# Kernel tuning notes

Measured on AMD Instinct MI355X. Metric: run time of the kernel, lower is better.

The kernel has to match this reference:

```python
import jax, jax.numpy as jnp
import numpy as np

E, B, DS, DA, H = 8, 16384, 32, 8, 128
SLOPE = 0.01  # torch leaky_relu default


def setup_inputs() -> dict:
    key = jax.random.key(0)
    ks = jax.random.split(key, 6)
    din = DS + DA
    return {
        "states": jax.random.normal(ks[0], (E, B, DS), jnp.float32),
        "actions": jax.random.normal(ks[1], (E, B, DA), jnp.float32),
        "W0": jax.random.normal(ks[2], (E, din, H), jnp.float32) / np.sqrt(din),
        "b0": jnp.zeros((E, H), jnp.float32),
        "W1": jax.random.normal(ks[3], (E, H, H), jnp.float32) / np.sqrt(H),
        "b1": jnp.zeros((E, H), jnp.float32),
        "W2": jax.random.normal(ks[4], (E, H, DS), jnp.float32) / np.sqrt(H),
        "b2": jnp.zeros((E, DS), jnp.float32),
    }


def reference(states, actions, W0, b0, W1, b1, W2, b2):
    # inp: (E_in, B, din); each input slice i is evaluated by every member j
    inp = jnp.concatenate([states, actions], axis=2)
    h = jax.nn.leaky_relu(
        jnp.einsum("ibd,jdh->ijbh", inp, W0) + b0[None, :, None, :], SLOPE
    )
    h = jax.nn.leaky_relu(
        jnp.einsum("ijbh,jhk->ijbk", h, W1) + b1[None, :, None, :], SLOPE
    )
    preds = jnp.einsum("ijbh,jhk->ijbk", h, W2) + b2[None, :, None, :]  # (E,E,B,DS)
    delta_mean = preds.mean(axis=0)           # (E, B, DS)
    var = preds.var(axis=0, ddof=1)           # torch.var default is unbiased
    next_state_mean = delta_mean + states
    return next_state_mean, var
```

## Files before the change

### kernel.cpp

```cpp
#include <hip/hip_runtime.h>
#include <hip/hip_bf16.h>


#define NE 8
#define NB 16384
#define DS 32
#define DA 8
#define HH 128
#define DIN 40
#define BT 64
#define SLOPE 0.01f

using bf16x8 = __attribute__((ext_vector_type(8))) short;
using f32x4  = __attribute__((ext_vector_type(4))) float;

__device__ __forceinline__ unsigned short f2bf(float f) {
    unsigned int u = __float_as_uint(f);
    u += 0x7FFFu + ((u >> 16) & 1u);
    return (unsigned short)(u >> 16);
}

__device__ __forceinline__ float lrelu(float x) { return fmaxf(x, SLOPE * x); }

__device__ __forceinline__ unsigned int pack2bf(float a, float b) {
    union { __hip_bfloat162 h; unsigned int u; } cv;
    cv.h = __float22bfloat162_rn(make_float2(a, b));
    return cv.u;
}

__device__ __forceinline__ int sin_idx(int row, int kb) {
    return row * 64 + ((kb ^ (row & 7)) << 3);
}
__device__ __forceinline__ int sh_idx(int row, int kb) {
    return row * 128 + ((kb ^ (row & 15)) << 3);
}

__global__ __launch_bounds__(256, 3)
void ens_mlp_kernel(const float* __restrict__ states,
                    const float* __restrict__ actions,
                    const float* __restrict__ W0g,
                    const float* __restrict__ b0g,
                    const float* __restrict__ W1g,
                    const float* __restrict__ b1g,
                    const float* __restrict__ W2g,
                    const float* __restrict__ b2g,
                    float* __restrict__ out)
{
    __shared__ __align__(16) unsigned short sIn[BT * 64];
    __shared__ __align__(16) unsigned short sHa[BT * 128];
    __shared__ __align__(16) unsigned short sHb[BT * 128];

    const int j    = blockIdx.x & 7;
    const int bt   = blockIdx.x >> 3;
    const int b0   = bt * BT;
    const int tid  = threadIdx.x;
    const int wave = tid >> 6;
    const int lane = tid & 63;
    const int q    = lane >> 4;
    const int l16  = lane & 15;
    const int fb   = 32 * wave;
    const int l2m  = 32 * (wave >> 1);
    const int l2n  = 16 * (wave & 1);

    {
        uint4 z; z.x = z.y = z.z = z.w = 0u;
        uint4* p = reinterpret_cast<uint4*>(&sIn[tid * 32]);
        p[0] = z; p[1] = z; p[2] = z; p[3] = z;
    }

    const float* W0j = W0g + j * (DIN * HH);
    const float* W1j = W1g + j * (HH * HH);
    const float* W2j = W2g + j * (HH * DS);

    bf16x8 w0f[2][2];
    bf16x8 w1f[4][2];
    bf16x8 w2f[4];
    float b1r[2][4];
    float b2s;

    #pragma unroll
    for (int ks = 0; ks < 2; ++ks)
      #pragma unroll
      for (int mt = 0; mt < 2; ++mt) {
        const int n = fb + mt * 16 + l16;
        #pragma unroll
        for (int t = 0; t < 8; ++t) {
          const int k = ks * 32 + q * 8 + t;
          const float v = (k < DIN) ? W0j[k * HH + n]
                        : (k == DIN ? b0g[j * HH + n] : 0.f);
          w0f[ks][mt][t] = (short)f2bf(v);
        }
      }
    #pragma unroll
    for (int ks = 0; ks < 4; ++ks)
      #pragma unroll
      for (int mt = 0; mt < 2; ++mt) {
        const int n = fb + mt * 16 + l16;
        #pragma unroll
        for (int t = 0; t < 8; ++t) {
          const int k = ks * 32 + q * 8 + t;
          w1f[ks][mt][t] = (short)f2bf(W1j[k * HH + n]);
        }
      }
    #pragma unroll
    for (int ks = 0; ks < 4; ++ks) {
        const int n = l2n + l16;
        #pragma unroll
        for (int t = 0; t < 8; ++t) {
          const int k = ks * 32 + q * 8 + t;
          w2f[ks][t] = (short)f2bf(W2j[k * DS + n]);
        }
    }
    #pragma unroll
    for (int mt = 0; mt < 2; ++mt)
      #pragma unroll
      for (int r = 0; r < 4; ++r)
        b1r[mt][r] = b1g[j * HH + fb + mt * 16 + q * 4 + r];
    b2s = b2g[j * DS + l2n + l16];

    float sa[2][4], sq[2][4];
    #pragma unroll
    for (int mt = 0; mt < 2; ++mt)
      #pragma unroll
      for (int r = 0; r < 4; ++r) { sa[mt][r] = 0.f; sq[mt][r] = 0.f; }

    const f32x4 z4 = {0.f, 0.f, 0.f, 0.f};

    const int srow = tid >> 2;
    const int scb  = tid & 3;
    const int soff = srow * DS + scb * 8;
    unsigned short* const sdst = &sIn[sin_idx(srow, scb)];
    unsigned short* const adst = &sIn[sin_idx(lane, 4)];

    __syncthreads();

    if (tid < BT) sIn[sin_idx(tid, 5)] = 0x3F80;

    {
        const float4* sp = reinterpret_cast<const float4*>(states + (size_t)b0 * DS + soff);
        const float4 f0 = sp[0], f1 = sp[1];
        uint4 pk;
        pk.x = pack2bf(f0.x, f0.y); pk.y = pack2bf(f0.z, f0.w);
        pk.z = pack2bf(f1.x, f1.y); pk.w = pack2bf(f1.z, f1.w);
        *reinterpret_cast<uint4*>(sdst) = pk;
        if (tid < BT) {
            const float4* ap = reinterpret_cast<const float4*>(actions + ((size_t)b0 + lane) * DA);
            const float4 a0 = ap[0], a1 = ap[1];
            uint4 apk;
            apk.x = pack2bf(a0.x, a0.y); apk.y = pack2bf(a0.z, a0.w);
            apk.z = pack2bf(a1.x, a1.y); apk.w = pack2bf(a1.z, a1.w);
            *reinterpret_cast<uint4*>(adst) = apk;
        }
    }
    __syncthreads();

    for (int i = 0; i < NE; ++i) {
        #pragma unroll
        for (int nh = 0; nh < 2; ++nh) {
            f32x4 acc[2][2];
            #pragma unroll
            for (int mt = 0; mt < 2; ++mt)
              #pragma unroll
              for (int nt = 0; nt < 2; ++nt) acc[mt][nt] = z4;
            #pragma unroll
            for (int ks = 0; ks < 2; ++ks) {
                bf16x8 bf[2];
                #pragma unroll
                for (int nt = 0; nt < 2; ++nt) {
                    const int row = nh * 32 + nt * 16 + l16;
                    bf[nt] = *(const bf16x8*)(&sIn[sin_idx(row, ks * 4 + q)]);
                }
                #pragma unroll
                for (int mt = 0; mt < 2; ++mt)
                  #pragma unroll
                  for (int nt = 0; nt < 2; ++nt)
                    acc[mt][nt] = __builtin_amdgcn_mfma_f32_16x16x32_bf16(
                        w0f[ks][mt], bf[nt], acc[mt][nt], 0, 0, 0);
            }
            #pragma unroll
            for (int mt = 0; mt < 2; ++mt)
              #pragma unroll
              for (int nt = 0; nt < 2; ++nt) {
                const int row = nh * 32 + nt * 16 + l16;
                const int blk = (fb >> 3) + mt * 2 + (q >> 1);
                const int idx = sh_idx(row, blk) + (q & 1) * 4;
                const float v0 = lrelu(acc[mt][nt][0]);
                const float v1 = lrelu(acc[mt][nt][1]);
                const float v2 = lrelu(acc[mt][nt][2]);
                const float v3 = lrelu(acc[mt][nt][3]);
                uint2 pk; pk.x = pack2bf(v0, v1); pk.y = pack2bf(v2, v3);
                *reinterpret_cast<uint2*>(&sHa[idx]) = pk;
              }
        }
        __syncthreads();

        if (i < NE - 1) {
            const float4* sp = reinterpret_cast<const float4*>(
                states + ((size_t)(i + 1) * NB + b0) * DS + soff);
            const float4 f0 = sp[0], f1 = sp[1];
            uint4 pk;
            pk.x = pack2bf(f0.x, f0.y); pk.y = pack2bf(f0.z, f0.w);
            pk.z = pack2bf(f1.x, f1.y); pk.w = pack2bf(f1.z, f1.w);
            *reinterpret_cast<uint4*>(sdst) = pk;
            if (tid < BT) {
                const float4* ap = reinterpret_cast<const float4*>(
                    actions + ((size_t)(i + 1) * NB + b0 + lane) * DA);
                const float4 a0 = ap[0], a1 = ap[1];
                uint4 apk;
                apk.x = pack2bf(a0.x, a0.y); apk.y = pack2bf(a0.z, a0.w);
                apk.z = pack2bf(a1.x, a1.y); apk.w = pack2bf(a1.z, a1.w);
                *reinterpret_cast<uint4*>(adst) = apk;
            }
        }

        #pragma unroll
        for (int nh = 0; nh < 2; ++nh) {
            f32x4 acc[2][2];
            #pragma unroll
            for (int mt = 0; mt < 2; ++mt)
              #pragma unroll
              for (int nt = 0; nt < 2; ++nt) acc[mt][nt] = z4;
            #pragma unroll
            for (int ks = 0; ks < 4; ++ks) {
                bf16x8 bf[2];
                #pragma unroll
                for (int nt = 0; nt < 2; ++nt) {
                    const int row = nh * 32 + nt * 16 + l16;
                    bf[nt] = *(const bf16x8*)(&sHa[sh_idx(row, ks * 4 + q)]);
                }
                #pragma unroll
                for (int mt = 0; mt < 2; ++mt)
                  #pragma unroll
                  for (int nt = 0; nt < 2; ++nt)
                    acc[mt][nt] = __builtin_amdgcn_mfma_f32_16x16x32_bf16(
                        w1f[ks][mt], bf[nt], acc[mt][nt], 0, 0, 0);
            }
            #pragma unroll
            for (int mt = 0; mt < 2; ++mt)
              #pragma unroll
              for (int nt = 0; nt < 2; ++nt) {
                const int row = nh * 32 + nt * 16 + l16;
                const int blk = (fb >> 3) + mt * 2 + (q >> 1);
                const int idx = sh_idx(row, blk) + (q & 1) * 4;
                const float v0 = lrelu(acc[mt][nt][0] + b1r[mt][0]);
                const float v1 = lrelu(acc[mt][nt][1] + b1r[mt][1]);
                const float v2 = lrelu(acc[mt][nt][2] + b1r[mt][2]);
                const float v3 = lrelu(acc[mt][nt][3] + b1r[mt][3]);
                uint2 pk; pk.x = pack2bf(v0, v1); pk.y = pack2bf(v2, v3);
                *reinterpret_cast<uint2*>(&sHb[idx]) = pk;
              }
        }
        __syncthreads();

        {
            f32x4 acc2[2];
            acc2[0] = z4; acc2[1] = z4;
            #pragma unroll
            for (int ks = 0; ks < 4; ++ks) {
                #pragma unroll
                for (int mt = 0; mt < 2; ++mt) {
                    const int row = l2m + 16 * mt + l16;
                    const bf16x8 a2 = *(const bf16x8*)(&sHb[sh_idx(row, ks * 4 + q)]);
                    acc2[mt] = __builtin_amdgcn_mfma_f32_16x16x32_bf16(
                        a2, w2f[ks], acc2[mt], 0, 0, 0);
                }
            }
            #pragma unroll
            for (int mt = 0; mt < 2; ++mt)
              #pragma unroll
              for (int r = 0; r < 4; ++r) {
                const float a = acc2[mt][r];
                sa[mt][r] += a;
                sq[mt][r] = fmaf(a, a, sq[mt][r]);
              }
        }
    }

    #pragma unroll
    for (int mt = 0; mt < 2; ++mt)
      #pragma unroll
      for (int r = 0; r < 4; ++r) {
        const int row = l2m + 16 * mt + q * 4 + r;
        const int col = l2n + l16;
        const size_t o = ((size_t)j * NB + b0 + row) * DS + col;
        const float b  = b2s;
        const float s  = sa[mt][r] + 8.f * b;
        const float s2 = sq[mt][r] + 2.f * b * sa[mt][r] + 8.f * b * b;
        out[o] = s * 0.125f + states[o];
        out[(size_t)NE * NB * DS + o] = (s2 - s * s * 0.125f) * (1.0f / 7.0f);
      }
}

extern "C" void kernel_launch(void* const* d_in, const int* in_sizes, int n_in,
                              void* d_out, int out_size, void* d_ws, size_t ws_size,
                              hipStream_t stream) {
    (void)in_sizes; (void)n_in; (void)d_ws; (void)ws_size; (void)out_size;
    const float* states  = (const float*)d_in[0];
    const float* actions = (const float*)d_in[1];
    const float* W0 = (const float*)d_in[2];
    const float* b0 = (const float*)d_in[3];
    const float* W1 = (const float*)d_in[4];
    const float* b1 = (const float*)d_in[5];
    const float* W2 = (const float*)d_in[6];
    const float* b2 = (const float*)d_in[7];
    float* out = (float*)d_out;
    dim3 grid(NE * (NB / BT));
    ens_mlp_kernel<<<grid, dim3(256), 0, stream>>>(states, actions, W0, b0, W1, b1, W2, b2, out);
}
```

Before: 161.7 us.

## Make blocks persistent over batch tiles and fold biases into accumulator init

The grid shrinks to 96 slots per ensemble member, and each block loops over several 64-row batch tiles. Per-member weights are converted to bf16 register fragments once per block and reused across tiles, which amortises the strided global weight loads and conversions that every block previously paid. The b0 and b1 biases now initialise the MFMA accumulators, replacing the ones-column trick for b0 and the per-element add for b1. In exchange, fewer blocks are in flight, and the tile count may not divide evenly across slots, which can leave a load-imbalance tail. The zero-initialisation of the input tile now has no barrier before other threads write into it, so correctness depends on the shared-memory layout.

Measured after the change: 153.9 us. 1.05x faster.

```diff
diff --git a/kernel.cpp b/kernel.cpp
--- a/kernel.cpp
+++ b/kernel.cpp
@@ -9,6 +9,7 @@
 #define HH 128
 #define DIN 40
 #define BT 64
+#define NSLOT 96
 #define SLOPE 0.01f
 
 using bf16x8 = __attribute__((ext_vector_type(8))) short;
@@ -51,8 +52,7 @@
     __shared__ __align__(16) unsigned short sHb[BT * 128];
 
     const int j    = blockIdx.x & 7;
-    const int bt   = blockIdx.x >> 3;
-    const int b0   = bt * BT;
+    const int slot = blockIdx.x >> 3;
     const int tid  = threadIdx.x;
     const int wave = tid >> 6;
     const int lane = tid & 63;
@@ -75,7 +75,7 @@
     bf16x8 w0f[2][2];
     bf16x8 w1f[4][2];
     bf16x8 w2f[4];
-    float b1r[2][4];
+    f32x4 b0v[2], b1v[2];
     float b2s;
 
     #pragma unroll
@@ -86,9 +86,7 @@
         #pragma unroll
         for (int t = 0; t < 8; ++t) {
           const int k = ks * 32 + q * 8 + t;
-          const float v = (k < DIN) ? W0j[k * HH + n]
-                        : (k == DIN ? b0g[j * HH + n] : 0.f);
-          w0f[ks][mt][t] = (short)f2bf(v);
+          w0f[ks][mt][t] = (short)((k < DIN) ? f2bf(W0j[k * HH + n]) : 0);
         }
       }
     #pragma unroll
@@ -114,15 +112,11 @@
     #pragma unroll
     for (int mt = 0; mt < 2; ++mt)
       #pragma unroll
-      for (int r = 0; r < 4; ++r)
-        b1r[mt][r] = b1g[j * HH + fb + mt * 16 + q * 4 + r];
+      for (int r = 0; r < 4; ++r) {
+        b0v[mt][r] = b0g[j * HH + fb + mt * 16 + q * 4 + r];
+        b1v[mt][r] = b1g[j * HH + fb + mt * 16 + q * 4 + r];
+      }
     b2s = b2g[j * DS + l2n + l16];
-
-    float sa[2][4], sq[2][4];
-    #pragma unroll
-    for (int mt = 0; mt < 2; ++mt)
-      #pragma unroll
-      for (int r = 0; r < 4; ++r) { sa[mt][r] = 0.f; sq[mt][r] = 0.f; }
 
     const f32x4 z4 = {0.f, 0.f, 0.f, 0.f};
 
@@ -132,71 +126,12 @@
     unsigned short* const sdst = &sIn[sin_idx(srow, scb)];
     unsigned short* const adst = &sIn[sin_idx(lane, 4)];
 
-    __syncthreads();
-
-    if (tid < BT) sIn[sin_idx(tid, 5)] = 0x3F80;
-
-    {
-        const float4* sp = reinterpret_cast<const float4*>(states + (size_t)b0 * DS + soff);
-        const float4 f0 = sp[0], f1 = sp[1];
-        uint4 pk;
-        pk.x = pack2bf(f0.x, f0.y); pk.y = pack2bf(f0.z, f0.w);
-        pk.z = pack2bf(f1.x, f1.y); pk.w = pack2bf(f1.z, f1.w);
-        *reinterpret_cast<uint4*>(sdst) = pk;
-        if (tid < BT) {
-            const float4* ap = reinterpret_cast<const float4*>(actions + ((size_t)b0 + lane) * DA);
-            const float4 a0 = ap[0], a1 = ap[1];
-            uint4 apk;
-            apk.x = pack2bf(a0.x, a0.y); apk.y = pack2bf(a0.z, a0.w);
-            apk.z = pack2bf(a1.x, a1.y); apk.w = pack2bf(a1.z, a1.w);
-            *reinterpret_cast<uint4*>(adst) = apk;
-        }
-    }
-    __syncthreads();
-
-    for (int i = 0; i < NE; ++i) {
-        #pragma unroll
-        for (int nh = 0; nh < 2; ++nh) {
-            f32x4 acc[2][2];
-            #pragma unroll
-            for (int mt = 0; mt < 2; ++mt)
-              #pragma unroll
-              for (int nt = 0; nt < 2; ++nt) acc[mt][nt] = z4;
-            #pragma unroll
-            for (int ks = 0; ks < 2; ++ks) {
-                bf16x8 bf[2];
-                #pragma unroll
-                for (int nt = 0; nt < 2; ++nt) {
-                    const int row = nh * 32 + nt * 16 + l16;
-                    bf[nt] = *(const bf16x8*)(&sIn[sin_idx(row, ks * 4 + q)]);
-                }
-                #pragma unroll
-                for (int mt = 0; mt < 2; ++mt)
-                  #pragma unroll
-                  for (int nt = 0; nt < 2; ++nt)
-                    acc[mt][nt] = __builtin_amdgcn_mfma_f32_16x16x32_bf16(
-                        w0f[ks][mt], bf[nt], acc[mt][nt], 0, 0, 0);
-            }
-            #pragma unroll
-            for (int mt = 0; mt < 2; ++mt)
-              #pragma unroll
-              for (int nt = 0; nt < 2; ++nt) {
-                const int row = nh * 32 + nt * 16 + l16;
-                const int blk = (fb >> 3) + mt * 2 + (q >> 1);
-                const int idx = sh_idx(row, blk) + (q & 1) * 4;
-                const float v0 = lrelu(acc[mt][nt][0]);
-                const float v1 = lrelu(acc[mt][nt][1]);
-                const float v2 = lrelu(acc[mt][nt][2]);
-                const float v3 = lrelu(acc[mt][nt][3]);
-                uint2 pk; pk.x = pack2bf(v0, v1); pk.y = pack2bf(v2, v3);
-                *reinterpret_cast<uint2*>(&sHa[idx]) = pk;
-              }
-        }
-        __syncthreads();
-
-        if (i < NE - 1) {
+    for (int bt = slot; bt < NB / BT; bt += NSLOT) {
+        const int b0 = bt * BT;
+
+        {
             const float4* sp = reinterpret_cast<const float4*>(
-                states + ((size_t)(i + 1) * NB + b0) * DS + soff);
+                states + (size_t)b0 * DS + soff);
             const float4 f0 = sp[0], f1 = sp[1];
             uint4 pk;
             pk.x = pack2bf(f0.x, f0.y); pk.y = pack2bf(f0.z, f0.w);
@@ -204,7 +139,7 @@
             *reinterpret_cast<uint4*>(sdst) = pk;
             if (tid < BT) {
                 const float4* ap = reinterpret_cast<const float4*>(
-                    actions + ((size_t)(i + 1) * NB + b0 + lane) * DA);
+                    actions + ((size_t)b0 + lane) * DA);
                 const float4 a0 = ap[0], a1 = ap[1];
                 uint4 apk;
                 apk.x = pack2bf(a0.x, a0.y); apk.y = pack2bf(a0.z, a0.w);
@@ -212,83 +147,150 @@
                 *reinterpret_cast<uint4*>(adst) = apk;
             }
         }
-
-        #pragma unroll
-        for (int nh = 0; nh < 2; ++nh) {
-            f32x4 acc[2][2];
+        __syncthreads();
+
+        float sa[2][4], sq[2][4];
+        #pragma unroll
+        for (int mt = 0; mt < 2; ++mt)
+          #pragma unroll
+          for (int r = 0; r < 4; ++r) { sa[mt][r] = 0.f; sq[mt][r] = 0.f; }
+
+        for (int i = 0; i < NE; ++i) {
             #pragma unroll
-            for (int mt = 0; mt < 2; ++mt)
-              #pragma unroll
-              for (int nt = 0; nt < 2; ++nt) acc[mt][nt] = z4;
+            for (int nh = 0; nh < 2; ++nh) {
+                f32x4 acc[2][2];
+                #pragma unroll
+                for (int mt = 0; mt < 2; ++mt)
+                  #pragma unroll
+                  for (int nt = 0; nt < 2; ++nt) acc[mt][nt] = b0v[mt];
+                #pragma unroll
+                for (int ks = 0; ks < 2; ++ks) {
+                    bf16x8 bf[2];
+                    #pragma unroll
+                    for (int nt = 0; nt < 2; ++nt) {
+                        const int row = nh * 32 + nt * 16 + l16;
+                        bf[nt] = *(const bf16x8*)(&sIn[sin_idx(row, ks * 4 + q)]);
+                    }
+                    #pragma unroll
+                    for (int mt = 0; mt < 2; ++mt)
+                      #pragma unroll
+                      for (int nt = 0; nt < 2; ++nt)
+                        acc[mt][nt] = __builtin_amdgcn_mfma_f32_16x16x32_bf16(
+                            w0f[ks][mt], bf[nt], acc[mt][nt], 0, 0, 0);
+                }
+                #pragma unroll
+                for (int mt = 0; mt < 2; ++mt)
+                  #pragma unroll
+                  for (int nt = 0; nt < 2; ++nt) {
+                    const int row = nh * 32 + nt * 16 + l16;
+                    const int blk = (fb >> 3) + mt * 2 + (q >> 1);
+                    const int idx = sh_idx(row, blk) + (q & 1) * 4;
+                    const float v0 = lrelu(acc[mt][nt][0]);
+                    const float v1 = lrelu(acc[mt][nt][1]);
+                    const float v2 = lrelu(acc[mt][nt][2]);
+                    const float v3 = lrelu(acc[mt][nt][3]);
+                    uint2 pk; pk.x = pack2bf(v0, v1); pk.y = pack2bf(v2, v3);
+                    *reinterpret_cast<uint2*>(&sHa[idx]) = pk;
+                  }
+            }
+            __syncthreads();
+
+            if (i < NE - 1) {
+                const float4* sp = reinterpret_cast<const float4*>(
+                    states + ((size_t)(i + 1) * NB + b0) * DS + soff);
+                const float4 f0 = sp[0], f1 = sp[1];
+                uint4 pk;
+                pk.x = pack2bf(f0.x, f0.y); pk.y = pack2bf(f0.z, f0.w);
+                pk.z = pack2bf(f1.x, f1.y); pk.w = pack2bf(f1.z, f1.w);
+                *reinterpret_cast<uint4*>(sdst) = pk;
+                if (tid < BT) {
+                    const float4* ap = reinterpret_cast<const float4*>(
+                        actions + ((size_t)(i + 1) * NB + b0 + lane) * DA);
+                    const float4 a0 = ap[0], a1 = ap[1];
+                    uint4 apk;
+                    apk.x = pack2bf(a0.x, a0.y); apk.y = pack2bf(a0.z, a0.w);
+                    apk.z = pack2bf(a1.x, a1.y); apk.w = pack2bf(a1.z, a1.w);
+                    *reinterpret_cast<uint4*>(adst) = apk;
+                }
+            }
+
             #pragma unroll
-            for (int ks = 0; ks < 4; ++ks) {
-                bf16x8 bf[2];
-                #pragma unroll
-                for (int nt = 0; nt < 2; ++nt) {
+            for (int nh = 0; nh < 2; ++nh) {
+                f32x4 acc[2][2];
+                #pragma unroll
+                for (int mt = 0; mt < 2; ++mt)
+                  #pragma unroll
+                  for (int nt = 0; nt < 2; ++nt) acc[mt][nt] = b1v[mt];
+                #pragma unroll
+                for (int ks = 0; ks < 4; ++ks) {
+                    bf16x8 bf[2];
+                    #pragma unroll
+                    for (int nt = 0; nt < 2; ++nt) {
+                        const int row = nh * 32 + nt * 16 + l16;
+                        bf[nt] = *(const bf16x8*)(&sHa[sh_idx(row, ks * 4 + q)]);
+                    }
+                    #pragma unroll
+                    for (int mt = 0; mt < 2; ++mt)
+                      #pragma unroll
+                      for (int nt = 0; nt < 2; ++nt)
+                        acc[mt][nt] = __builtin_amdgcn_mfma_f32_16x16x32_bf16(
+                            w1f[ks][mt], bf[nt], acc[mt][nt], 0, 0, 0);
+                }
+                #pragma unroll
+                for (int mt = 0; mt < 2; ++mt)
+                  #pragma unroll
+                  for (int nt = 0; nt < 2; ++nt) {
                     const int row = nh * 32 + nt * 16 + l16;
-                    bf[nt] = *(const bf16x8*)(&sHa[sh_idx(row, ks * 4 + q)]);
+                    const int blk = (fb >> 3) + mt * 2 + (q >> 1);
+                    const int idx = sh_idx(row, blk) + (q & 1) * 4;
+                    const float v0 = lrelu(acc[mt][nt][0]);
+                    const float v1 = lrelu(acc[mt][nt][1]);
+                    const float v2 = lrelu(acc[mt][nt][2]);
+                    const float v3 = lrelu(acc[mt][nt][3]);
+                    uint2 pk; pk.x = pack2bf(v0, v1); pk.y = pack2bf(v2, v3);
+                    *reinterpret_cast<uint2*>(&sHb[idx]) = pk;
+                  }
+            }
+            __syncthreads();
+
+            {
+                f32x4 acc2[2];
+                acc2[0] = z4; acc2[1] = z4;
+                #pragma unroll
+                for (int ks = 0; ks < 4; ++ks) {
+                    #pragma unroll
+                    for (int mt = 0; mt < 2; ++mt) {
+                        const int row = l2m + 16 * mt + l16;
+                        const bf16x8 a2 = *(const bf16x8*)(&sHb[sh_idx(row, ks * 4 + q)]);
+                        acc2[mt] = __builtin_amdgcn_mfma_f32_16x16x32_bf16(
+                            a2, w2f[ks], acc2[mt], 0, 0, 0);
+                    }
                 }
                 #pragma unroll
                 for (int mt = 0; mt < 2; ++mt)
                   #pragma unroll
-                  for (int nt = 0; nt < 2; ++nt)
-                    acc[mt][nt] = __builtin_amdgcn_mfma_f32_16x16x32_bf16(
-                        w1f[ks][mt], bf[nt], acc[mt][nt], 0, 0, 0);
-            }
-            #pragma unroll
-            for (int mt = 0; mt < 2; ++mt)
-              #pragma unroll
-              for (int nt = 0; nt < 2; ++nt) {
-                const int row = nh * 32 + nt * 16 + l16;
-                const int blk = (fb >> 3) + mt * 2 + (q >> 1);
-                const int idx = sh_idx(row, blk) + (q & 1) * 4;
-                const float v0 = lrelu(acc[mt][nt][0] + b1r[mt][0]);
-                const float v1 = lrelu(acc[mt][nt][1] + b1r[mt][1]);
-                const float v2 = lrelu(acc[mt][nt][2] + b1r[mt][2]);
-                const float v3 = lrelu(acc[mt][nt][3] + b1r[mt][3]);
-                uint2 pk; pk.x = pack2bf(v0, v1); pk.y = pack2bf(v2, v3);
-                *reinterpret_cast<uint2*>(&sHb[idx]) = pk;
-              }
-        }
-        __syncthreads();
-
-        {
-            f32x4 acc2[2];
-            acc2[0] = z4; acc2[1] = z4;
-            #pragma unroll
-            for (int ks = 0; ks < 4; ++ks) {
-                #pragma unroll
-                for (int mt = 0; mt < 2; ++mt) {
-                    const int row = l2m + 16 * mt + l16;
-                    const bf16x8 a2 = *(const bf16x8*)(&sHb[sh_idx(row, ks * 4 + q)]);
-                    acc2[mt] = __builtin_amdgcn_mfma_f32_16x16x32_bf16(
-                        a2, w2f[ks], acc2[mt], 0, 0, 0);
-                }
-            }
-            #pragma unroll
-            for (int mt = 0; mt < 2; ++mt)
-              #pragma unroll
-              for (int r = 0; r < 4; ++r) {
-                const float a = acc2[mt][r];
-                sa[mt][r] += a;
-                sq[mt][r] = fmaf(a, a, sq[mt][r]);
-              }
-        }
+                  for (int r = 0; r < 4; ++r) {
+                    const float a = acc2[mt][r];
+                    sa[mt][r] += a;
+                    sq[mt][r] = fmaf(a, a, sq[mt][r]);
+                  }
+            }
+        }
+
+        #pragma unroll
+        for (int mt = 0; mt < 2; ++mt)
+          #pragma unroll
+          for (int r = 0; r < 4; ++r) {
+            const int row = l2m + 16 * mt + q * 4 + r;
+            const int col = l2n + l16;
+            const size_t o = ((size_t)j * NB + b0 + row) * DS + col;
+            const float b  = b2s;
+            const float s  = sa[mt][r] + 8.f * b;
+            const float s2 = sq[mt][r] + 2.f * b * sa[mt][r] + 8.f * b * b;
+            out[o] = s * 0.125f + states[o];
+            out[(size_t)NE * NB * DS + o] = (s2 - s * s * 0.125f) * (1.0f / 7.0f);
+          }
     }
-
-    #pragma unroll
-    for (int mt = 0; mt < 2; ++mt)
-      #pragma unroll
-      for (int r = 0; r < 4; ++r) {
-        const int row = l2m + 16 * mt + q * 4 + r;
-        const int col = l2n + l16;
-        const size_t o = ((size_t)j * NB + b0 + row) * DS + col;
-        const float b  = b2s;
-        const float s  = sa[mt][r] + 8.f * b;
-        const float s2 = sq[mt][r] + 2.f * b * sa[mt][r] + 8.f * b * b;
-        out[o] = s * 0.125f + states[o];
-        out[(size_t)NE * NB * DS + o] = (s2 - s * s * 0.125f) * (1.0f / 7.0f);
-      }
 }
 
 extern "C" void kernel_launch(void* const* d_in, const int* in_sizes, int n_in,
@@ -304,6 +306,6 @@
     const float* W2 = (const float*)d_in[6];
     const float* b2 = (const float*)d_in[7];
     float* out = (float*)d_out;
-    dim3 grid(NE * (NB / BT));
+    dim3 grid(8 * NSLOT);
     ens_mlp_kernel<<<grid, dim3(256), 0, stream>>>(states, actions, W0, b0, W1, b1, W2, b2, out);
 }
```
